# Optimization experiments

Hardware: AMD Instinct MI355X
Metric: run time of the kernel (lower is better)

## Reference

```python
import jax, jax.numpy as jnp
import numpy as np

N = 131072   # atoms
D = 384      # aev dim
E = 4        # experts (elements)
H1, H2, H3 = 256, 192, 160


def setup_inputs() -> dict:
    key = jax.random.key(0)
    ks = jax.random.split(key, 12)
    s = 0.05
    inp = {
        "aev": jax.random.normal(ks[0], (N, D), dtype=jnp.float32),
        "index": jax.random.randint(ks[1], (N,), 0, E),
        # stacked per-expert MLP weights [E, in, out]
        "W1": jax.random.normal(ks[2], (E, D, H1), dtype=jnp.float32) * s,
        "b1": jax.random.normal(ks[3], (E, H1), dtype=jnp.float32) * s,
        "W2": jax.random.normal(ks[4], (E, H1, H2), dtype=jnp.float32) * s,
        "b2": jax.random.normal(ks[5], (E, H2), dtype=jnp.float32) * s,
        "W3": jax.random.normal(ks[6], (E, H2, H3), dtype=jnp.float32) * s,
        "b3": jax.random.normal(ks[7], (E, H3), dtype=jnp.float32) * s,
        "W4": jax.random.normal(ks[8], (E, H3, 1), dtype=jnp.float32) * s,
        "b4": jax.random.normal(ks[9], (E, 1), dtype=jnp.float32) * s,
        "alphas": jnp.ones((E,), dtype=jnp.float32),
        "shifts": jnp.array([-0.5, -37.8, -54.5, -75.0], dtype=jnp.float32),
    }
    return inp


def reference(aev, index, W1, b1, W2, b2, W3, b3, W4, b4, alphas, shifts):
    # Run all E expert MLPs densely on all atoms, then select per-atom by index.
    # Same math per selected expert as torch masked dispatch/combine.
    h = jax.nn.celu(jnp.einsum('nd,edh->enh', aev, W1) + b1[:, None, :])
    h = jax.nn.celu(jnp.einsum('enh,ehk->enk', h, W2) + b2[:, None, :])
    h = jax.nn.celu(jnp.einsum('enk,ekm->enm', h, W3) + b3[:, None, :])
    y = (jnp.einsum('enm,emo->eno', h, W4) + b4[:, None, :])[..., 0]  # [E, N]
    y = y * alphas[:, None] + shifts[:, None]                         # shifted nets
    out = jnp.take_along_axis(y, index[None, :], axis=0)[0]           # [N]
    return out
```

## Files before the change

### kernel.cpp

```cpp
#include <hip/hip_runtime.h>
#include <hip/hip_bf16.h>

#define NATOMS 131072
#define DIM    384
#define NE     4
#define H1N    256
#define H2N    192
#define H3N    160
#define BM     64
#define NTH    256
#define NTILES (NATOMS/BM + NE)

typedef __attribute__((ext_vector_type(8))) short bf16x8;
typedef __attribute__((ext_vector_type(4))) float f32x4;
typedef __attribute__((ext_vector_type(4))) int   i32x4;
typedef __attribute__((ext_vector_type(2))) int   i32x2;

#define WS_META   0
#define WS_TABLE  64
#define WS_PERM   (WS_TABLE + NTILES*16)
#define WS_WT1    ((WS_PERM + NATOMS*4 + 255) & ~255)
#define SZ_WT1    (NE*H1N*DIM*2)
#define WS_WT2    (WS_WT1 + SZ_WT1)
#define SZ_WT2    (NE*H2N*H1N*2)
#define WS_WT3    (WS_WT2 + SZ_WT2)
#define SZ_WT3    (NE*H3N*H2N*2 + 4096)

#define L_SLOT(i) ((i)*16384)
#define L_H       32768
#define LDS_TOTAL (L_H + BM*528)

static __device__ __forceinline__ unsigned short f2bf(float f) {
  union { __hip_bfloat16 h; unsigned short u; } v;
  v.h = __float2bfloat16(f);
  return v.u;
}
static __device__ __forceinline__ unsigned pack2(float a, float b) {
  union { __hip_bfloat162 h2; unsigned u; } v;
  v.h2 = __float22bfloat162_rn(make_float2(a, b));
  return v.u;
}
static __device__ __forceinline__ float celu1(float x) {
  return x > 0.f ? x : (__expf(x) - 1.f);
}
static __device__ __forceinline__ bf16x8 cvt8(f32x4 a, f32x4 b) {
  union { bf16x8 v; unsigned u[4]; } r;
  r.u[0] = pack2(a.x, a.y); r.u[1] = pack2(a.z, a.w);
  r.u[2] = pack2(b.x, b.y); r.u[3] = pack2(b.z, b.w);
  return r.v;
}

#define SCHEDB __builtin_amdgcn_sched_barrier(0)
#define VMWAIT(N) do { asm volatile("s_waitcnt vmcnt(" #N ")" ::: "memory"); SCHEDB; } while(0)
#define LGKM0  do { asm volatile("s_waitcnt lgkmcnt(0)" ::: "memory"); SCHEDB; } while(0)
#define BARRIER do { __builtin_amdgcn_s_barrier(); SCHEDB; } while(0)

#define GLDS16(gp, lp) __builtin_amdgcn_global_load_lds( \
    (const __attribute__((address_space(1))) unsigned int*)(gp), \
    (__attribute__((address_space(3))) unsigned int*)(lp), 16, 0, 0)

__global__ void k_zero(int* meta) {
  if (threadIdx.x < 16) meta[threadIdx.x] = 0;
}

__global__ void k_wprep(const float* __restrict__ W1, const float* __restrict__ W2,
                        const float* __restrict__ W3,
                        unsigned short* __restrict__ wt1,
                        unsigned short* __restrict__ wt2,
                        unsigned short* __restrict__ wt3) {
  __shared__ float t[32][33];
  int b = blockIdx.x;
  const float* W; unsigned short* wt; int K, NN, ntiles, idx;
  if (b < 384)      { W = W1; wt = wt1; K = 384; NN = 256; ntiles = 8; idx = b; }
  else if (b < 576) { W = W2; wt = wt2; K = 256; NN = 192; ntiles = 6; idx = b - 384; }
  else              { W = W3; wt = wt3; K = 192; NN = 160; ntiles = 5; idx = b - 576; }
  int per_e = (K / 32) * ntiles;
  int e  = idx / per_e;
  int r  = idx % per_e;
  int kt = r / ntiles, nt = r % ntiles;

  int row = threadIdx.x >> 3, c4 = (threadIdx.x & 7) * 4;
  float4 v = *(const float4*)(W + ((size_t)(e * K + kt * 32 + row) * NN + nt * 32 + c4));
  t[row][c4 + 0] = v.x; t[row][c4 + 1] = v.y;
  t[row][c4 + 2] = v.z; t[row][c4 + 3] = v.w;
  __syncthreads();

  int n = threadIdx.x >> 3, k4 = (threadIdx.x & 7) * 4;
  unsigned short o[4];
  o[0] = f2bf(t[k4 + 0][n]); o[1] = f2bf(t[k4 + 1][n]);
  o[2] = f2bf(t[k4 + 2][n]); o[3] = f2bf(t[k4 + 3][n]);
  i32x2 p; p.x = (int)(o[0] | ((unsigned)o[1] << 16));
  p.y = (int)(o[2] | ((unsigned)o[3] << 16));
  *(i32x2*)(wt + ((size_t)(e * (K / 32) + kt) * NN + nt * 32 + n) * 32 + k4) = p;
}

__global__ void k_hist(const int* __restrict__ index, int* __restrict__ meta) {
  __shared__ int h[NE];
  int t = threadIdx.x;
  if (t < NE) h[t] = 0;
  __syncthreads();
  int b0 = blockIdx.x * 1024;
  #pragma unroll
  for (int j = 0; j < 4; ++j) atomicAdd(&h[index[b0 + t + j*256]], 1);
  __syncthreads();
  if (t < NE) atomicAdd(&meta[t], h[t]);
}

__global__ void k_plan(int* __restrict__ meta, i32x4* __restrict__ table) {
  __shared__ int off[NE + 1], nt[NE + 1];
  if (threadIdx.x == 0) {
    int o = 0, t = 0;
    for (int e = 0; e < NE; ++e) {
      off[e] = o; nt[e] = t;
      o += meta[e];
      t += (meta[e] + BM - 1) / BM;
      meta[4 + e] = off[e];
    }
    off[NE] = o; nt[NE] = t;
  }
  __syncthreads();
  for (int i = threadIdx.x; i < NTILES; i += blockDim.x) {
    i32x4 v = {0, 0, 0, 0};
    for (int e = 0; e < NE; ++e) {
      if (i >= nt[e] && i < nt[e + 1]) {
        int local = i - nt[e];
        int cnt = off[e + 1] - off[e];
        int rem = cnt - local * BM;
        v.x = e; v.y = off[e] + local * BM; v.z = rem < BM ? rem : BM;
      }
    }
    table[i] = v;
  }
}

__global__ void k_scatter(const int* __restrict__ index, int* __restrict__ meta,
                          int* __restrict__ perm) {
  __shared__ int h[NE], base[NE];
  int t = threadIdx.x;
  if (t < NE) h[t] = 0;
  __syncthreads();
  int b0 = blockIdx.x * 1024;
  int eIdx[4];
  #pragma unroll
  for (int j = 0; j < 4; ++j) {
    eIdx[j] = index[b0 + t + j*256];
    atomicAdd(&h[eIdx[j]], 1);
  }
  __syncthreads();
  if (t < NE) { base[t] = atomicAdd(&meta[4 + t], h[t]); h[t] = 0; }
  __syncthreads();
  #pragma unroll
  for (int j = 0; j < 4; ++j) {
    int e = eIdx[j];
    int slot = atomicAdd(&h[e], 1);
    perm[base[e] + slot] = b0 + t + j*256;
  }
}

__launch_bounds__(NTH, 2)
__global__ void k_mlp(const float* __restrict__ aev,
                      const unsigned short* __restrict__ wt1,
                      const unsigned short* __restrict__ wt2,
                      const unsigned short* __restrict__ wt3,
                      const float* __restrict__ b1g,
                      const float* __restrict__ b2g,
                      const float* __restrict__ b3g,
                      const float* __restrict__ w4g,
                      const float* __restrict__ b4g,
                      const float* __restrict__ alpg,
                      const float* __restrict__ shfg,
                      const int* __restrict__ perm,
                      const i32x4* __restrict__ table,
                      float* __restrict__ out)
{
  extern __shared__ char smem[];

  i32x4 tt = table[blockIdx.x];
  const int e = tt.x, start = tt.y, len = tt.z;
  if (len == 0) return;

  const int tid = threadIdx.x;
  const int l   = tid & 63;
  const int w   = tid >> 6;
  const int l15 = l & 15;
  const int lg  = l >> 4;

  const char* w1c = (const char*)wt1 + (size_t)e * (12 * 16384);
  const char* w2c = (const char*)wt2 + (size_t)e * (8 * 12288);
  const char* w3c = (const char*)wt3 + (size_t)e * (6 * 10240);

#define STAGE4(GB, SLOT) do { \
    const char* _g = (GB) + w * 4096 + l * 16; \
    char* _l = smem + L_SLOT(SLOT) + w * 4096; \
    GLDS16(_g, _l); GLDS16(_g + 1024, _l + 1024); \
    GLDS16(_g + 2048, _l + 2048); GLDS16(_g + 3072, _l + 3072); \
    SCHEDB; \
  } while (0)
#define STAGE3(GB, SLOT) do { \
    const char* _g = (GB) + w * 3072 + l * 16; \
    char* _l = smem + L_SLOT(SLOT) + w * 3072; \
    GLDS16(_g, _l); GLDS16(_g + 1024, _l + 1024); GLDS16(_g + 2048, _l + 2048); \
    SCHEDB; \
  } while (0)

  const float* xp[4];
  #pragma unroll
  for (int mf = 0; mf < 4; ++mf) {
    int r = mf * 16 + l15;
    int ar = (r < len) ? perm[start + r] : 0;
    xp[mf] = aev + (size_t)ar * DIM + lg * 8;
  }

  STAGE4(w1c, 0);
  f32x4 xq[2][4][2];
  #pragma unroll
  for (int s = 0; s < 2; ++s)
    #pragma unroll
    for (int mf = 0; mf < 4; ++mf) {
      xq[s][mf][0] = *(const f32x4*)(xp[mf] + s * 32);
      xq[s][mf][1] = *(const f32x4*)(xp[mf] + s * 32 + 4);
    }
  SCHEDB;

  f32x4 acc[4][4];
  #pragma unroll
  for (int a = 0; a < 4; ++a)
    #pragma unroll
    for (int b = 0; b < 4; ++b)
      acc[a][b] = f32x4{0.f, 0.f, 0.f, 0.f};
  float4 b1v[4];

  #pragma unroll
  for (int kk = 0; kk < 12; ++kk) {
    if (kk < 11) VMWAIT(8); else VMWAIT(0);
    BARRIER;
    if (kk == 11) {
      #pragma unroll
      for (int ni = 0; ni < 4; ++ni)
        b1v[ni] = *(const float4*)(b1g + e * H1N + w * 64 + ni * 16 + lg * 4);
      SCHEDB;
    }
    if (kk < 11) STAGE4(w1c + (kk + 1) * 16384, (kk + 1) & 1);
    else         STAGE3(w2c, 0);
    bf16x8 bx[4];
    #pragma unroll
    for (int mf = 0; mf < 4; ++mf)
      bx[mf] = cvt8(xq[kk & 1][mf][0], xq[kk & 1][mf][1]);
    if (kk < 10) {
      #pragma unroll
      for (int mf = 0; mf < 4; ++mf) {
        xq[kk & 1][mf][0] = *(const f32x4*)(xp[mf] + (kk + 2) * 32);
        xq[kk & 1][mf][1] = *(const f32x4*)(xp[mf] + (kk + 2) * 32 + 4);
      }
      SCHEDB;
    }
    #pragma unroll
    for (int ni = 0; ni < 4; ++ni) {
      bf16x8 af = *(const bf16x8*)(smem + L_SLOT(kk & 1)
                                   + (w * 64 + ni * 16 + l15) * 64 + lg * 16);
      #pragma unroll
      for (int mf = 0; mf < 4; ++mf)
        acc[ni][mf] = __builtin_amdgcn_mfma_f32_16x16x32_bf16(
            af, bx[mf], acc[ni][mf], 0, 0, 0);
    }
  }

  #pragma unroll
  for (int ni = 0; ni < 4; ++ni) {
    const int nb = w * 64 + ni * 16 + lg * 4;
    #pragma unroll
    for (int mf = 0; mf < 4; ++mf) {
      f32x4 v = acc[ni][mf];
      i32x2 p;
      p.x = (int)pack2(celu1(v.x + b1v[ni].x), celu1(v.y + b1v[ni].y));
      p.y = (int)pack2(celu1(v.z + b1v[ni].z), celu1(v.w + b1v[ni].w));
      *(i32x2*)(smem + L_H + (mf * 16 + l15) * 528 + nb * 2) = p;
    }
  }
  LGKM0; BARRIER;

  f32x4 acc2[3][4];
  #pragma unroll
  for (int a = 0; a < 3; ++a)
    #pragma unroll
    for (int b = 0; b < 4; ++b)
      acc2[a][b] = f32x4{0.f, 0.f, 0.f, 0.f};
  float4 b2v[3];

  #pragma unroll
  for (int c = 0; c < 8; ++c) {
    VMWAIT(0);
    BARRIER;
    if (c == 7) {
      #pragma unroll
      for (int ni = 0; ni < 3; ++ni)
        b2v[ni] = *(const float4*)(b2g + e * H2N + w * 48 + ni * 16 + lg * 4);
      SCHEDB;
    }
    if (c < 7) STAGE3(w2c + (c + 1) * 12288, (c + 1) & 1);
    else       STAGE3(w3c, 0);
    bf16x8 bh[4];
    #pragma unroll
    for (int mf = 0; mf < 4; ++mf)
      bh[mf] = *(const bf16x8*)(smem + L_H + (mf * 16 + l15) * 528 + c * 64 + lg * 16);
    #pragma unroll
    for (int ni = 0; ni < 3; ++ni) {
      bf16x8 af = *(const bf16x8*)(smem + L_SLOT(c & 1)
                                   + (w * 48 + ni * 16 + l15) * 64 + lg * 16);
      #pragma unroll
      for (int mf = 0; mf < 4; ++mf)
        acc2[ni][mf] = __builtin_amdgcn_mfma_f32_16x16x32_bf16(
            af, bh[mf], acc2[ni][mf], 0, 0, 0);
    }
  }

  BARRIER;
  #pragma unroll
  for (int ni = 0; ni < 3; ++ni) {
    const int nb = w * 48 + ni * 16 + lg * 4;
    #pragma unroll
    for (int mf = 0; mf < 4; ++mf) {
      f32x4 v = acc2[ni][mf];
      i32x2 p;
      p.x = (int)pack2(celu1(v.x + b2v[ni].x), celu1(v.y + b2v[ni].y));
      p.y = (int)pack2(celu1(v.z + b2v[ni].z), celu1(v.w + b2v[ni].w));
      *(i32x2*)(smem + L_H + (mf * 16 + l15) * 400 + nb * 2) = p;
    }
  }
  LGKM0; BARRIER;

  const int nf3 = (w < 2) ? 3 : 2;
  f32x4 acc3[3][4];
  #pragma unroll
  for (int a = 0; a < 3; ++a)
    #pragma unroll
    for (int b = 0; b < 4; ++b)
      acc3[a][b] = f32x4{0.f, 0.f, 0.f, 0.f};

  #pragma unroll
  for (int u = 0; u < 6; ++u) {
    VMWAIT(0);
    BARRIER;
    if (u < 5) STAGE3(w3c + (u + 1) * 10240, (u + 1) & 1);
    bf16x8 bh[4];
    #pragma unroll
    for (int mf = 0; mf < 4; ++mf)
      bh[mf] = *(const bf16x8*)(smem + L_H + (mf * 16 + l15) * 400 + u * 64 + lg * 16);
    #pragma unroll
    for (int ni = 0; ni < 3; ++ni) {
      if (ni < nf3) {
        bf16x8 af = *(const bf16x8*)(smem + L_SLOT(u & 1)
                                     + ((w + ni * 4) * 16 + l15) * 64 + lg * 16);
        #pragma unroll
        for (int mf = 0; mf < 4; ++mf)
          acc3[ni][mf] = __builtin_amdgcn_mfma_f32_16x16x32_bf16(
              af, bh[mf], acc3[ni][mf], 0, 0, 0);
      }
    }
  }

  BARRIER;
  float part[4] = {0.f, 0.f, 0.f, 0.f};
  #pragma unroll
  for (int ni = 0; ni < 3; ++ni) {
    if (ni < nf3) {
      const int nb = (w + ni * 4) * 16 + lg * 4;
      float4 b3v = *(const float4*)(b3g + e * H3N + nb);
      float4 w4v = *(const float4*)(w4g + e * H3N + nb);
      #pragma unroll
      for (int mf = 0; mf < 4; ++mf) {
        f32x4 v = acc3[ni][mf];
        part[mf] += celu1(v.x + b3v.x) * w4v.x + celu1(v.y + b3v.y) * w4v.y
                  + celu1(v.z + b3v.z) * w4v.z + celu1(v.w + b3v.w) * w4v.w;
      }
    }
  }
  #pragma unroll
  for (int mf = 0; mf < 4; ++mf) {
    part[mf] += __shfl_xor(part[mf], 16);
    part[mf] += __shfl_xor(part[mf], 32);
  }
  float* pb = (float*)smem;
  if (lg == 0) {
    #pragma unroll
    for (int mf = 0; mf < 4; ++mf) pb[w * 64 + mf * 16 + l15] = part[mf];
  }
  LGKM0; BARRIER;
  if (tid < BM && tid < len) {
    float s = pb[tid] + pb[64 + tid] + pb[128 + tid] + pb[192 + tid];
    float y = (s + b4g[e]) * alpg[e] + shfg[e];
    out[perm[start + tid]] = y;
  }
#undef STAGE4
#undef STAGE3
}

extern "C" void kernel_launch(void* const* d_in, const int* in_sizes, int n_in,
                              void* d_out, int out_size, void* d_ws, size_t ws_size,
                              hipStream_t stream) {
  (void)in_sizes; (void)n_in; (void)out_size; (void)ws_size;
  const float* aev    = (const float*)d_in[0];
  const int*   index  = (const int*)d_in[1];
  const float* W1     = (const float*)d_in[2];
  const float* b1     = (const float*)d_in[3];
  const float* W2     = (const float*)d_in[4];
  const float* b2     = (const float*)d_in[5];
  const float* W3     = (const float*)d_in[6];
  const float* b3     = (const float*)d_in[7];
  const float* W4     = (const float*)d_in[8];
  const float* b4     = (const float*)d_in[9];
  const float* alphas = (const float*)d_in[10];
  const float* shifts = (const float*)d_in[11];
  float* out = (float*)d_out;
  char* ws = (char*)d_ws;

  int*   meta  = (int*)(ws + WS_META);
  i32x4* table = (i32x4*)(ws + WS_TABLE);
  int*   perm  = (int*)(ws + WS_PERM);
  unsigned short* wt1 = (unsigned short*)(ws + WS_WT1);
  unsigned short* wt2 = (unsigned short*)(ws + WS_WT2);
  unsigned short* wt3 = (unsigned short*)(ws + WS_WT3);

  hipFuncSetAttribute((const void*)k_mlp,
                      hipFuncAttributeMaxDynamicSharedMemorySize, LDS_TOTAL);

  k_zero<<<1, 64, 0, stream>>>(meta);
  k_wprep<<<696, 256, 0, stream>>>(W1, W2, W3, wt1, wt2, wt3);
  k_hist<<<NATOMS/1024, 256, 0, stream>>>(index, meta);
  k_plan<<<1, 256, 0, stream>>>(meta, table);
  k_scatter<<<NATOMS/1024, 256, 0, stream>>>(index, meta, perm);
  k_mlp<<<NTILES, NTH, LDS_TOTAL, stream>>>(
      aev, wt1, wt2, wt3, b1, b2, b3, W4, b4, alphas, shifts, perm, table, out);
}
```

Baseline: 427.8 us.

## Double atom tile to 128 with 8 waves and stage gathered inputs via LDS DMA

```diff
diff --git a/kernel.cpp b/kernel.cpp
--- a/kernel.cpp
+++ b/kernel.cpp
@@ -7,8 +7,8 @@
 #define H1N    256
 #define H2N    192
 #define H3N    160
-#define BM     64
-#define NTH    256
+#define BM     128
+#define NTH    512
 #define NTILES (NATOMS/BM + NE)
 
 typedef __attribute__((ext_vector_type(8))) short bf16x8;
@@ -20,14 +20,15 @@
 #define WS_TABLE  64
 #define WS_PERM   (WS_TABLE + NTILES*16)
 #define WS_WT1    ((WS_PERM + NATOMS*4 + 255) & ~255)
-#define SZ_WT1    (NE*H1N*DIM*2)
+#define SZ_WT1    (NE*12*16384)
 #define WS_WT2    (WS_WT1 + SZ_WT1)
-#define SZ_WT2    (NE*H2N*H1N*2)
+#define SZ_WT2    (NE*8*16384)
 #define WS_WT3    (WS_WT2 + SZ_WT2)
-#define SZ_WT3    (NE*H3N*H2N*2 + 4096)
-
-#define L_SLOT(i) ((i)*16384)
-#define L_H       32768
+#define SZ_WT3    (NE*6*16384)
+
+#define L_X   0
+#define L_W   49152
+#define L_H   81920
 #define LDS_TOTAL (L_H + BM*528)
 
 static __device__ __forceinline__ unsigned short f2bf(float f) {
@@ -59,6 +60,17 @@
     (const __attribute__((address_space(1))) unsigned int*)(gp), \
     (__attribute__((address_space(3))) unsigned int*)(lp), 16, 0, 0)
 
+#define STAGE_TILE(gbase, lbase) do { \
+    GLDS16((gbase) + tid * 16,        (lbase) + tid * 16); \
+    GLDS16((gbase) + 8192 + tid * 16, (lbase) + 8192 + tid * 16); \
+    SCHEDB; \
+  } while (0)
+#define STAGE_X(kk, rs) do { \
+    GLDS16(xsrc + (kk) * 128,      smem + L_X + (rs) * 16384 + tid * 16); \
+    GLDS16(xsrc + (kk) * 128 + 64, smem + L_X + (rs) * 16384 + 8192 + tid * 16); \
+    SCHEDB; \
+  } while (0)
+
 __global__ void k_zero(int* meta) {
   if (threadIdx.x < 16) meta[threadIdx.x] = 0;
 }
@@ -68,30 +80,26 @@
                         unsigned short* __restrict__ wt1,
                         unsigned short* __restrict__ wt2,
                         unsigned short* __restrict__ wt3) {
-  __shared__ float t[32][33];
   int b = blockIdx.x;
-  const float* W; unsigned short* wt; int K, NN, ntiles, idx;
-  if (b < 384)      { W = W1; wt = wt1; K = 384; NN = 256; ntiles = 8; idx = b; }
-  else if (b < 576) { W = W2; wt = wt2; K = 256; NN = 192; ntiles = 6; idx = b - 384; }
-  else              { W = W3; wt = wt3; K = 192; NN = 160; ntiles = 5; idx = b - 576; }
-  int per_e = (K / 32) * ntiles;
-  int e  = idx / per_e;
-  int r  = idx % per_e;
-  int kt = r / ntiles, nt = r % ntiles;
-
-  int row = threadIdx.x >> 3, c4 = (threadIdx.x & 7) * 4;
-  float4 v = *(const float4*)(W + ((size_t)(e * K + kt * 32 + row) * NN + nt * 32 + c4));
-  t[row][c4 + 0] = v.x; t[row][c4 + 1] = v.y;
-  t[row][c4 + 2] = v.z; t[row][c4 + 3] = v.w;
-  __syncthreads();
-
-  int n = threadIdx.x >> 3, k4 = (threadIdx.x & 7) * 4;
-  unsigned short o[4];
-  o[0] = f2bf(t[k4 + 0][n]); o[1] = f2bf(t[k4 + 1][n]);
-  o[2] = f2bf(t[k4 + 2][n]); o[3] = f2bf(t[k4 + 3][n]);
-  i32x2 p; p.x = (int)(o[0] | ((unsigned)o[1] << 16));
-  p.y = (int)(o[2] | ((unsigned)o[3] << 16));
-  *(i32x2*)(wt + ((size_t)(e * (K / 32) + kt) * NN + nt * 32 + n) * 32 + k4) = p;
+  const float* W; unsigned short* base; int K, NN, e, kt;
+  if (b < 48)      { e = b / 12; kt = b % 12; W = W1; base = wt1 + ((size_t)(e * 12 + kt)) * 8192; K = 384; NN = 256; }
+  else if (b < 80) { int i = b - 48; e = i / 8; kt = i % 8; W = W2; base = wt2 + ((size_t)(e * 8 + kt)) * 8192; K = 256; NN = 192; }
+  else             { int i = b - 80; e = i / 6; kt = i % 6; W = W3; base = wt3 + ((size_t)(e * 6 + kt)) * 8192; K = 192; NN = 160; }
+  int n = threadIdx.x;
+  if (n >= NN) return;
+  float v[32];
+  #pragma unroll
+  for (int k = 0; k < 32; ++k)
+    v[k] = W[((size_t)(e * K + kt * 32 + k)) * NN + n];
+  #pragma unroll
+  for (int g = 0; g < 4; ++g) {
+    i32x4 p;
+    p.x = (int)pack2(v[g*8+0], v[g*8+1]);
+    p.y = (int)pack2(v[g*8+2], v[g*8+3]);
+    p.z = (int)pack2(v[g*8+4], v[g*8+5]);
+    p.w = (int)pack2(v[g*8+6], v[g*8+7]);
+    *(i32x4*)(base + n * 32 + g * 8) = p;
+  }
 }
 
 __global__ void k_hist(const int* __restrict__ index, int* __restrict__ meta) {
@@ -159,9 +167,9 @@
 
 __launch_bounds__(NTH, 2)
 __global__ void k_mlp(const float* __restrict__ aev,
-                      const unsigned short* __restrict__ wt1,
-                      const unsigned short* __restrict__ wt2,
-                      const unsigned short* __restrict__ wt3,
+                      const char* __restrict__ wt1c,
+                      const char* __restrict__ wt2c,
+                      const char* __restrict__ wt3c,
                       const float* __restrict__ b1g,
                       const float* __restrict__ b2g,
                       const float* __restrict__ b3g,
@@ -182,45 +190,39 @@
   const int tid = threadIdx.x;
   const int l   = tid & 63;
   const int w   = tid >> 6;
+  const int wq  = w & 3;
+  const int mh  = w >> 2;
   const int l15 = l & 15;
   const int lg  = l >> 4;
 
-  const char* w1c = (const char*)wt1 + (size_t)e * (12 * 16384);
-  const char* w2c = (const char*)wt2 + (size_t)e * (8 * 12288);
-  const char* w3c = (const char*)wt3 + (size_t)e * (6 * 10240);
-
-#define STAGE4(GB, SLOT) do { \
-    const char* _g = (GB) + w * 4096 + l * 16; \
-    char* _l = smem + L_SLOT(SLOT) + w * 4096; \
-    GLDS16(_g, _l); GLDS16(_g + 1024, _l + 1024); \
-    GLDS16(_g + 2048, _l + 2048); GLDS16(_g + 3072, _l + 3072); \
-    SCHEDB; \
-  } while (0)
-#define STAGE3(GB, SLOT) do { \
-    const char* _g = (GB) + w * 3072 + l * 16; \
-    char* _l = smem + L_SLOT(SLOT) + w * 3072; \
-    GLDS16(_g, _l); GLDS16(_g + 1024, _l + 1024); GLDS16(_g + 2048, _l + 2048); \
-    SCHEDB; \
-  } while (0)
-
-  const float* xp[4];
-  #pragma unroll
-  for (int mf = 0; mf < 4; ++mf) {
-    int r = mf * 16 + l15;
-    int ar = (r < len) ? perm[start + r] : 0;
-    xp[mf] = aev + (size_t)ar * DIM + lg * 8;
-  }
-
-  STAGE4(w1c, 0);
-  f32x4 xq[2][4][2];
-  #pragma unroll
-  for (int s = 0; s < 2; ++s)
-    #pragma unroll
-    for (int mf = 0; mf < 4; ++mf) {
-      xq[s][mf][0] = *(const f32x4*)(xp[mf] + s * 32);
-      xq[s][mf][1] = *(const f32x4*)(xp[mf] + s * 32 + 4);
-    }
-  SCHEDB;
+  float4 b1v[4], b2v[3], b3v[3], w4v[3];
+  #pragma unroll
+  for (int ni = 0; ni < 4; ++ni)
+    b1v[ni] = *(const float4*)(b1g + e * H1N + wq * 64 + ni * 16 + lg * 4);
+  #pragma unroll
+  for (int ni = 0; ni < 3; ++ni)
+    b2v[ni] = *(const float4*)(b2g + e * H2N + wq * 48 + ni * 16 + lg * 4);
+  const int nf3 = (wq < 2) ? 3 : 2;
+  int frag3[3];
+  frag3[0] = wq * 2; frag3[1] = wq * 2 + 1; frag3[2] = (wq < 2) ? (8 + wq) : 0;
+  #pragma unroll
+  for (int i = 0; i < 3; ++i) {
+    b3v[i] = *(const float4*)(b3g + e * H3N + frag3[i] * 16 + lg * 4);
+    w4v[i] = *(const float4*)(w4g + e * H3N + frag3[i] * 16 + lg * 4);
+  }
+  const float b4s = b4g[e], alps = alpg[e], shfs = shfg[e];
+
+  const int a0 = tid & 127;
+  const int row = (a0 < len) ? perm[start + a0] : perm[start];
+  const char* xsrc = (const char*)aev + (size_t)row * (DIM * 4) + (tid >> 7) * 16;
+
+  const char* w1c = wt1c + (size_t)e * (12 * 16384);
+  const char* w2c = wt2c + (size_t)e * (8 * 16384);
+  const char* w3c = wt3c + (size_t)e * (6 * 16384);
+
+  STAGE_TILE(w1c, smem + L_W);
+  STAGE_X(0, 0);
+  STAGE_X(1, 1);
 
   f32x4 acc[4][4];
   #pragma unroll
@@ -228,53 +230,47 @@
     #pragma unroll
     for (int b = 0; b < 4; ++b)
       acc[a][b] = f32x4{0.f, 0.f, 0.f, 0.f};
-  float4 b1v[4];
 
   #pragma unroll
   for (int kk = 0; kk < 12; ++kk) {
-    if (kk < 11) VMWAIT(8); else VMWAIT(0);
+    VMWAIT(2);
     BARRIER;
-    if (kk == 11) {
-      #pragma unroll
-      for (int ni = 0; ni < 4; ++ni)
-        b1v[ni] = *(const float4*)(b1g + e * H1N + w * 64 + ni * 16 + lg * 4);
-      SCHEDB;
-    }
-    if (kk < 11) STAGE4(w1c + (kk + 1) * 16384, (kk + 1) & 1);
-    else         STAGE3(w2c, 0);
+    if (kk < 11) STAGE_TILE(w1c + (kk + 1) * 16384, smem + L_W + ((kk + 1) & 1) * 16384);
+    if (kk <= 9)       STAGE_X(kk + 2, (kk + 2) % 3);
+    else if (kk == 10) STAGE_TILE(w2c, smem + L_X);
+    else               STAGE_TILE(w2c + 16384, smem + L_X + 16384);
+
+    const char* xs = smem + L_X + (kk % 3) * 16384;
     bf16x8 bx[4];
     #pragma unroll
-    for (int mf = 0; mf < 4; ++mf)
-      bx[mf] = cvt8(xq[kk & 1][mf][0], xq[kk & 1][mf][1]);
-    if (kk < 10) {
-      #pragma unroll
-      for (int mf = 0; mf < 4; ++mf) {
-        xq[kk & 1][mf][0] = *(const f32x4*)(xp[mf] + (kk + 2) * 32);
-        xq[kk & 1][mf][1] = *(const f32x4*)(xp[mf] + (kk + 2) * 32 + 4);
-      }
-      SCHEDB;
-    }
-    #pragma unroll
-    for (int ni = 0; ni < 4; ++ni) {
-      bf16x8 af = *(const bf16x8*)(smem + L_SLOT(kk & 1)
-                                   + (w * 64 + ni * 16 + l15) * 64 + lg * 16);
+    for (int mf = 0; mf < 4; ++mf) {
+      const int atom = mh * 64 + mf * 16 + l15;
+      f32x4 lo = *(const f32x4*)(xs + (2 * lg) * 2048 + atom * 16);
+      f32x4 hi = *(const f32x4*)(xs + (2 * lg + 1) * 2048 + atom * 16);
+      bx[mf] = cvt8(lo, hi);
+    }
+    const char* wsl = smem + L_W + (kk & 1) * 16384;
+    #pragma unroll
+    for (int nf = 0; nf < 4; ++nf) {
+      bf16x8 af = *(const bf16x8*)(wsl + (wq * 64 + nf * 16 + l15) * 64 + lg * 16);
       #pragma unroll
       for (int mf = 0; mf < 4; ++mf)
-        acc[ni][mf] = __builtin_amdgcn_mfma_f32_16x16x32_bf16(
-            af, bx[mf], acc[ni][mf], 0, 0, 0);
+        acc[nf][mf] = __builtin_amdgcn_mfma_f32_16x16x32_bf16(
+            af, bx[mf], acc[nf][mf], 0, 0, 0);
     }
   }
 
   #pragma unroll
   for (int ni = 0; ni < 4; ++ni) {
-    const int nb = w * 64 + ni * 16 + lg * 4;
+    const int nb = wq * 64 + ni * 16 + lg * 4;
     #pragma unroll
     for (int mf = 0; mf < 4; ++mf) {
+      const int atom = mh * 64 + mf * 16 + l15;
       f32x4 v = acc[ni][mf];
       i32x2 p;
       p.x = (int)pack2(celu1(v.x + b1v[ni].x), celu1(v.y + b1v[ni].y));
       p.y = (int)pack2(celu1(v.z + b1v[ni].z), celu1(v.w + b1v[ni].w));
-      *(i32x2*)(smem + L_H + (mf * 16 + l15) * 528 + nb * 2) = p;
+      *(i32x2*)(smem + L_H + atom * 528 + nb * 2) = p;
     }
   }
   LGKM0; BARRIER;
@@ -285,51 +281,48 @@
     #pragma unroll
     for (int b = 0; b < 4; ++b)
       acc2[a][b] = f32x4{0.f, 0.f, 0.f, 0.f};
-  float4 b2v[3];
 
   #pragma unroll
   for (int c = 0; c < 8; ++c) {
-    VMWAIT(0);
+    VMWAIT(2);
     BARRIER;
-    if (c == 7) {
-      #pragma unroll
-      for (int ni = 0; ni < 3; ++ni)
-        b2v[ni] = *(const float4*)(b2g + e * H2N + w * 48 + ni * 16 + lg * 4);
-      SCHEDB;
-    }
-    if (c < 7) STAGE3(w2c + (c + 1) * 12288, (c + 1) & 1);
-    else       STAGE3(w3c, 0);
+    if (c < 6)       STAGE_TILE(w2c + (c + 2) * 16384, smem + L_X + ((c + 2) % 3) * 16384);
+    else if (c == 6) STAGE_TILE(w3c, smem + L_W);
+    else             STAGE_TILE(w3c + 16384, smem + L_W + 16384);
+
     bf16x8 bh[4];
     #pragma unroll
-    for (int mf = 0; mf < 4; ++mf)
-      bh[mf] = *(const bf16x8*)(smem + L_H + (mf * 16 + l15) * 528 + c * 64 + lg * 16);
-    #pragma unroll
-    for (int ni = 0; ni < 3; ++ni) {
-      bf16x8 af = *(const bf16x8*)(smem + L_SLOT(c & 1)
-                                   + (w * 48 + ni * 16 + l15) * 64 + lg * 16);
+    for (int mf = 0; mf < 4; ++mf) {
+      const int atom = mh * 64 + mf * 16 + l15;
+      bh[mf] = *(const bf16x8*)(smem + L_H + atom * 528 + c * 64 + lg * 16);
+    }
+    const char* wsl = smem + L_X + (c % 3) * 16384;
+    #pragma unroll
+    for (int nf = 0; nf < 3; ++nf) {
+      bf16x8 af = *(const bf16x8*)(wsl + (wq * 48 + nf * 16 + l15) * 64 + lg * 16);
       #pragma unroll
       for (int mf = 0; mf < 4; ++mf)
-        acc2[ni][mf] = __builtin_amdgcn_mfma_f32_16x16x32_bf16(
-            af, bh[mf], acc2[ni][mf], 0, 0, 0);
+        acc2[nf][mf] = __builtin_amdgcn_mfma_f32_16x16x32_bf16(
+            af, bh[mf], acc2[nf][mf], 0, 0, 0);
     }
   }
 
   BARRIER;
   #pragma unroll
   for (int ni = 0; ni < 3; ++ni) {
-    const int nb = w * 48 + ni * 16 + lg * 4;
+    const int nb = wq * 48 + ni * 16 + lg * 4;
     #pragma unroll
     for (int mf = 0; mf < 4; ++mf) {
+      const int atom = mh * 64 + mf * 16 + l15;
       f32x4 v = acc2[ni][mf];
       i32x2 p;
       p.x = (int)pack2(celu1(v.x + b2v[ni].x), celu1(v.y + b2v[ni].y));
       p.y = (int)pack2(celu1(v.z + b2v[ni].z), celu1(v.w + b2v[ni].w));
-      *(i32x2*)(smem + L_H + (mf * 16 + l15) * 400 + nb * 2) = p;
+      *(i32x2*)(smem + L_H + atom * 400 + nb * 2) = p;
     }
   }
   LGKM0; BARRIER;
 
-  const int nf3 = (w < 2) ? 3 : 2;
   f32x4 acc3[3][4];
   #pragma unroll
   for (int a = 0; a < 3; ++a)
@@ -339,22 +332,29 @@
 
   #pragma unroll
   for (int u = 0; u < 6; ++u) {
-    VMWAIT(0);
+    if (u < 5) { VMWAIT(2); } else { VMWAIT(0); }
     BARRIER;
-    if (u < 5) STAGE3(w3c + (u + 1) * 10240, (u + 1) & 1);
+    if (u < 4) {
+      const int s = (u + 2) % 3;
+      char* dst = (s == 0) ? (smem + L_W) : (s == 1) ? (smem + L_W + 16384) : (smem + L_X);
+      STAGE_TILE(w3c + (u + 2) * 16384, dst);
+    }
     bf16x8 bh[4];
     #pragma unroll
-    for (int mf = 0; mf < 4; ++mf)
-      bh[mf] = *(const bf16x8*)(smem + L_H + (mf * 16 + l15) * 400 + u * 64 + lg * 16);
-    #pragma unroll
-    for (int ni = 0; ni < 3; ++ni) {
-      if (ni < nf3) {
-        bf16x8 af = *(const bf16x8*)(smem + L_SLOT(u & 1)
-                                     + ((w + ni * 4) * 16 + l15) * 64 + lg * 16);
+    for (int mf = 0; mf < 4; ++mf) {
+      const int atom = mh * 64 + mf * 16 + l15;
+      bh[mf] = *(const bf16x8*)(smem + L_H + atom * 400 + u * 64 + lg * 16);
+    }
+    const int s = u % 3;
+    const char* wsl = (s == 0) ? (smem + L_W) : (s == 1) ? (smem + L_W + 16384) : (smem + L_X);
+    #pragma unroll
+    for (int i = 0; i < 3; ++i) {
+      if (i < nf3) {
+        bf16x8 af = *(const bf16x8*)(wsl + (frag3[i] * 16 + l15) * 64 + lg * 16);
         #pragma unroll
         for (int mf = 0; mf < 4; ++mf)
-          acc3[ni][mf] = __builtin_amdgcn_mfma_f32_16x16x32_bf16(
-              af, bh[mf], acc3[ni][mf], 0, 0, 0);
+          acc3[i][mf] = __builtin_amdgcn_mfma_f32_16x16x32_bf16(
+              af, bh[mf], acc3[i][mf], 0, 0, 0);
       }
     }
   }
@@ -362,16 +362,15 @@
   BARRIER;
   float part[4] = {0.f, 0.f, 0.f, 0.f};
   #pragma unroll
-  for (int ni = 0; ni < 3; ++ni) {
-    if (ni < nf3) {
-      const int nb = (w + ni * 4) * 16 + lg * 4;
-      float4 b3v = *(const float4*)(b3g + e * H3N + nb);
-      float4 w4v = *(const float4*)(w4g + e * H3N + nb);
+  for (int i = 0; i < 3; ++i) {
+    if (i < nf3) {
       #pragma unroll
       for (int mf = 0; mf < 4; ++mf) {
-        f32x4 v = acc3[ni][mf];
-        part[mf] += celu1(v.x + b3v.x) * w4v.x + celu1(v.y + b3v.y) * w4v.y
-                  + celu1(v.z + b3v.z) * w4v.z + celu1(v.w + b3v.w) * w4v.w;
+        f32x4 v = acc3[i][mf];
+        part[mf] += celu1(v.x + b3v[i].x) * w4v[i].x
+                  + celu1(v.y + b3v[i].y) * w4v[i].y
+                  + celu1(v.z + b3v[i].z) * w4v[i].z
+                  + celu1(v.w + b3v[i].w) * w4v[i].w;
       }
     }
   }
@@ -380,19 +379,18 @@
     part[mf] += __shfl_xor(part[mf], 16);
     part[mf] += __shfl_xor(part[mf], 32);
   }
-  float* pb = (float*)smem;
+  float* pb = (float*)(smem + L_X);
   if (lg == 0) {
     #pragma unroll
     for (int mf = 0; mf < 4; ++mf) pb[w * 64 + mf * 16 + l15] = part[mf];
   }
   LGKM0; BARRIER;
   if (tid < BM && tid < len) {
-    float s = pb[tid] + pb[64 + tid] + pb[128 + tid] + pb[192 + tid];
-    float y = (s + b4g[e]) * alpg[e] + shfg[e];
-    out[perm[start + tid]] = y;
-  }
-#undef STAGE4
-#undef STAGE3
+    const int hb = (tid >> 6) * 4, lo = tid & 63;
+    float s = pb[(hb + 0) * 64 + lo] + pb[(hb + 1) * 64 + lo]
+            + pb[(hb + 2) * 64 + lo] + pb[(hb + 3) * 64 + lo];
+    out[perm[start + tid]] = (s + b4s) * alps + shfs;
+  }
 }
 
 extern "C" void kernel_launch(void* const* d_in, const int* in_sizes, int n_in,
@@ -425,10 +423,11 @@
                       hipFuncAttributeMaxDynamicSharedMemorySize, LDS_TOTAL);
 
   k_zero<<<1, 64, 0, stream>>>(meta);
-  k_wprep<<<696, 256, 0, stream>>>(W1, W2, W3, wt1, wt2, wt3);
+  k_wprep<<<104, 256, 0, stream>>>(W1, W2, W3, wt1, wt2, wt3);
   k_hist<<<NATOMS/1024, 256, 0, stream>>>(index, meta);
   k_plan<<<1, 256, 0, stream>>>(meta, table);
   k_scatter<<<NATOMS/1024, 256, 0, stream>>>(index, meta, perm);
   k_mlp<<<NTILES, NTH, LDS_TOTAL, stream>>>(
-      aev, wt1, wt2, wt3, b1, b2, b3, W4, b4, alphas, shifts, perm, table, out);
-}
+      aev, (const char*)wt1, (const char*)wt2, (const char*)wt3,
+      b1, b2, b3, W4, b4, alphas, shifts, perm, table, out);
+}
```

Result: faster. 395.6 us (-7.5%).
